# Kernel tuning notes

Measured on AMD Instinct MI355X. Metric: run time of the kernel, lower is better.

Reference implementation:

```python
import jax, jax.numpy as jnp
import numpy as np

B, L, NS, D, M = 64, 200, 1000, 128, 50


def setup_inputs() -> dict:
    key = jax.random.key(0)
    ks = jax.random.split(key, 12)
    s = np.sqrt(2.0 / D).astype(np.float32)  # kaiming_normal scale for Mk/Mv0
    lw = np.sqrt(1.0 / D).astype(np.float32)
    return {
        "skills": jax.random.randint(ks[0], (B, L), 0, NS),
        "responses": jax.random.randint(ks[1], (B, L), 0, 2),
        "k_emb": jax.random.normal(ks[2], (NS, D), jnp.float32) * 0.02,
        "v_emb": jax.random.normal(ks[3], (2 * NS, D), jnp.float32) * 0.02,
        "Mk": jax.random.normal(ks[4], (M, D), jnp.float32) * s,
        "Mv0": jax.random.normal(ks[5], (M, D), jnp.float32) * s,
        "e_W": jax.random.normal(ks[6], (D, D), jnp.float32) * lw,
        "e_b": jnp.zeros((D,), jnp.float32),
        "a_W": jax.random.normal(ks[7], (D, D), jnp.float32) * lw,
        "a_b": jnp.zeros((D,), jnp.float32),
        "f_W": jax.random.normal(ks[8], (D, 2 * D), jnp.float32) * np.sqrt(1.0 / (2 * D)).astype(np.float32),
        "f_b": jnp.zeros((D,), jnp.float32),
        "p_W": jax.random.normal(ks[9], (1, D), jnp.float32) * lw,
        "p_b": jnp.zeros((1,), jnp.float32),
    }


def _dkvmn_forward(skills, responses, k_emb, v_emb, Mk, Mv0,
                   e_W, e_b, a_W, a_b, f_W, f_b, p_W, p_b):
    masked_r = responses * (responses > -1).astype(responses.dtype)
    x = skills + NS * masked_r                      # [B,L] combined (skill,response) id
    k = k_emb[skills]                               # [B,L,D]
    v = v_emb[x]                                    # [B,L,D]
    w = jax.nn.softmax(jnp.einsum('bld,md->blm', k, Mk), axis=-1)  # [B,L,M]
    e = jax.nn.sigmoid(v @ e_W.T + e_b)             # erase  [B,L,D]
    a = jnp.tanh(v @ a_W.T + a_b)                   # add    [B,L,D]

    def step(Mvt, wea):
        wt, et, at = wea                            # [B,M], [B,D], [B,D]
        u = wt[:, :, None]                          # [B,M,1]
        new = Mvt * (1.0 - u * et[:, None, :]) + u * at[:, None, :]
        return new, Mvt                             # emit PRE-update state (Mv[:, :-1])

    Mv_init = jnp.broadcast_to(Mv0[None], (B, M, D))
    _, Mv_pre = jax.lax.scan(
        step, Mv_init,
        (w.transpose(1, 0, 2), e.transpose(1, 0, 2), a.transpose(1, 0, 2)))
    # Mv_pre: [L,B,M,D]; weighted read of pre-update memory
    read = jnp.einsum('blm,lbmd->bld', w, Mv_pre)   # [B,L,D]
    f = jnp.tanh(jnp.concatenate([read, k], axis=-1) @ f_W.T + f_b)  # [B,L,D]
    p = jax.nn.sigmoid(f @ p_W.T + p_b)[..., 0]     # [B,L] (dropout off: eval)
    return p[:, 1:]                                 # pred, [B,L-1]


def reference(skills, responses, k_emb, v_emb, Mk, Mv0,
              e_W, e_b, a_W, a_b, f_W, f_b, p_W, p_b):
    return _dkvmn_forward(skills, responses, k_emb, v_emb, Mk, Mv0,
                          e_W, e_b, a_W, a_b, f_W, f_b, p_W, p_b)
```

## Files before the change

kernel.cpp:

```cpp
#include <hip/hip_runtime.h>
#include <hip/hip_bf16.h>

#define Bb 64
#define Ll 200
#define NSs 1000
#define Dd 128
#define Mm 50

__device__ __forceinline__ float bcast_lane(float v, int l) {
    return __int_as_float(__builtin_amdgcn_readlane(__float_as_int(v), l));
}

__global__ void __launch_bounds__(256) kern_wea(
        const int* __restrict__ skills,
        const int* __restrict__ responses,
        const float* __restrict__ k_emb,
        const float* __restrict__ v_emb,
        const float* __restrict__ Mk,
        const float* __restrict__ e_W, const float* __restrict__ e_b,
        const float* __restrict__ a_W, const float* __restrict__ a_b,
        float* __restrict__ w_out,
        float* __restrict__ e_out, float* __restrict__ a_out) {
    __shared__ float smem[12672];
    int tid = threadIdx.x;

    if (blockIdx.x >= 400) {
        int blk = blockIdx.x - 400;
        float (*mk)[Dd + 4] = (float(*)[Dd + 4])smem;
        float (*kr)[Dd + 4] = (float(*)[Dd + 4])(smem + 6600);

        for (int lin = tid; lin < (Mm * Dd) / 4; lin += 256) {
            float4 f = ((const float4*)Mk)[lin];
            *(float4*)&mk[lin >> 5][(lin & 31) * 4] = f;
        }
        for (int lin = tid; lin < 16 * 32; lin += 256) {
            int r  = lin >> 5;
            int c4 = lin & 31;
            int bl = blk * 16 + r;
            float4 f = ((const float4*)(k_emb + (size_t)skills[bl] * Dd))[c4];
            *(float4*)&kr[r][c4 * 4] = f;
        }
        __syncthreads();

        int wave = tid >> 6, lane = tid & 63;
        int mmr  = (lane < Mm) ? lane : 0;
        float acc[4] = {0.f, 0.f, 0.f, 0.f};
#pragma unroll 2
        for (int q = 0; q < 32; ++q) {
            float4 mkv = *(const float4*)&mk[mmr][q * 4];
#pragma unroll
            for (int i = 0; i < 4; ++i) {
                float4 kv = *(const float4*)&kr[wave * 4 + i][q * 4];
                acc[i] = fmaf(mkv.x, kv.x, acc[i]);
                acc[i] = fmaf(mkv.y, kv.y, acc[i]);
                acc[i] = fmaf(mkv.z, kv.z, acc[i]);
                acc[i] = fmaf(mkv.w, kv.w, acc[i]);
            }
        }
#pragma unroll
        for (int i = 0; i < 4; ++i) {
            float logit = (lane < Mm) ? acc[i] : -1e30f;
            float mx = logit;
            for (int off = 32; off > 0; off >>= 1) mx = fmaxf(mx, __shfl_down(mx, off));
            mx = __shfl(mx, 0);
            float ex = (lane < Mm) ? expf(logit - mx) : 0.f;
            float sm = ex;
            for (int off = 32; off > 0; off >>= 1) sm += __shfl_down(sm, off);
            sm = __shfl(sm, 0);
            int bl = blk * 16 + wave * 4 + i;
            if (lane < Mm) w_out[(size_t)bl * Mm + lane] = ex / sm;
        }
        return;
    }

    int blk = blockIdx.x;
    float (*vt)[Dd + 4] = (float(*)[Dd + 4])smem;
    float (*wt)[Dd + 4] = (float(*)[Dd + 4])(smem + 4224);

#pragma unroll
    for (int i = 0; i < 4; ++i) {
        int lin = i * 256 + tid;
        int r   = lin >> 5;
        int c4  = lin & 31;
        int bl  = blk * 32 + r;
        int rr  = responses[bl];
        int x   = skills[bl] + NSs * ((rr > -1) ? rr : 0);
        float4 f = ((const float4*)(v_emb + (size_t)x * Dd))[c4];
        *(float4*)&vt[r][c4 * 4] = f;
    }
    __syncthreads();

    int wave = tid >> 6, lane = tid & 63;
    int pg = lane >> 3, og = lane & 7;

    for (int s = 0; s < 4; ++s) {
        int base_row = wave * 64 + s * 16;
        bool is_e    = base_row < 128;
        const float* W = is_e ? e_W : a_W;
        int wrow0 = is_e ? base_row : base_row - 128;

#pragma unroll
        for (int i = 0; i < 8; ++i) {
            int lin = i * 64 + lane;
            int r   = lin >> 5;
            int c4  = lin & 31;
            float4 f = ((const float4*)(W + (size_t)(wrow0 + r) * Dd))[c4];
            *(float4*)&wt[wave * 16 + r][c4 * 4] = f;
        }

        float acc[4][2] = {};
#pragma unroll 2
        for (int q = 0; q < 32; ++q) {
            float4 av[4], bv[2];
#pragma unroll
            for (int i = 0; i < 4; ++i) av[i] = *(const float4*)&vt[pg + 8 * i][q * 4];
#pragma unroll
            for (int j = 0; j < 2; ++j) bv[j] = *(const float4*)&wt[wave * 16 + og + 8 * j][q * 4];
#pragma unroll
            for (int i = 0; i < 4; ++i)
#pragma unroll
                for (int j = 0; j < 2; ++j) {
                    acc[i][j] = fmaf(av[i].x, bv[j].x, acc[i][j]);
                    acc[i][j] = fmaf(av[i].y, bv[j].y, acc[i][j]);
                    acc[i][j] = fmaf(av[i].z, bv[j].z, acc[i][j]);
                    acc[i][j] = fmaf(av[i].w, bv[j].w, acc[i][j]);
                }
        }

        float* dst = is_e ? e_out : a_out;
#pragma unroll
        for (int j = 0; j < 2; ++j) {
            int row = wrow0 + og + 8 * j;
            float bias = (is_e ? e_b : a_b)[row];
#pragma unroll
            for (int i = 0; i < 4; ++i) {
                int bl = blk * 32 + pg + 8 * i;
                float v = acc[i][j] + bias;
                dst[(size_t)bl * Dd + row] = is_e ? (1.f / (1.f + expf(-v))) : tanhf(v);
            }
        }
    }
}

#define PQ_LOAD(S, tt) do { int _t = (tt);                                   \
    if (_t < T) { size_t _bl = blBase + _t;                                  \
        w##S = (lane < Mm) ? w_ws[_bl * Mm + lane] : 0.f;                    \
        e##S = e_ws[_bl * Dd + d];  a##S = a_ws[_bl * Dd + d]; } } while (0)

#define PQ_BODY(S) do {                                                      \
    _Pragma("unroll")                                                        \
    for (int m = 0; m < Mm; ++m) {                                           \
        float wm = bcast_lane(w##S, m);                                      \
        float A  = fmaf(-wm, e##S, 1.f);                                     \
        Q[m] = fmaf(A, Q[m], wm * a##S);                                     \
        P[m] *= A; } } while (0)

__global__ void __launch_bounds__(128) kern_scan_pq(
        const float* __restrict__ w_ws,
        const float* __restrict__ e_ws,
        const float* __restrict__ a_ws,
        float* __restrict__ P_ws, float* __restrict__ Q_ws,
        int C, int T) {
    int b = blockIdx.x / C, c = blockIdx.x % C;
    int d = threadIdx.x;
    int lane = d & 63;
    float P[Mm], Q[Mm];
#pragma unroll
    for (int m = 0; m < Mm; ++m) { P[m] = 1.f; Q[m] = 0.f; }

    size_t blBase = (size_t)b * Ll + (size_t)c * T;
    float w0 = 0.f, e0 = 0.f, a0 = 0.f;
    float w1 = 0.f, e1 = 0.f, a1 = 0.f;
    float w2 = 0.f, e2 = 0.f, a2 = 0.f;
    PQ_LOAD(0, 0);
    PQ_LOAD(1, 1);
    for (int tt = 0; tt < T; tt += 3) {
        PQ_LOAD(2, tt + 2);  PQ_BODY(0);
        if (tt + 1 < T) { PQ_LOAD(0, tt + 3);  PQ_BODY(1); }
        if (tt + 2 < T) { PQ_LOAD(1, tt + 4);  PQ_BODY(2); }
    }
    size_t base = ((size_t)(b * C + c)) * (Mm * Dd) + d;
#pragma unroll
    for (int m = 0; m < Mm; ++m) {
        P_ws[base + m * Dd] = P[m];
        Q_ws[base + m * Dd] = Q[m];
    }
}

template <int CC>
__global__ void kern_scan_comb_t(
        const float* __restrict__ Mv0,
        const float* __restrict__ P_ws, const float* __restrict__ Q_ws,
        float* __restrict__ S_ws) {
    int idx = blockIdx.x * 256 + threadIdx.x;
    int b   = idx / (Mm * Dd);
    int md  = idx % (Mm * Dd);
    float Pr[CC - 1], Qr[CC - 1];
#pragma unroll
    for (int c = 0; c < CC - 1; ++c) {
        size_t pq = ((size_t)(b * CC + c)) * (Mm * Dd) + md;
        Pr[c] = P_ws[pq];
        Qr[c] = Q_ws[pq];
    }
    float s = Mv0[md];
#pragma unroll
    for (int c = 0; c < CC - 1; ++c) {
        s = fmaf(Pr[c], s, Qr[c]);
        S_ws[((size_t)(b * (CC - 1) + c)) * (Mm * Dd) + md] = s;
    }
}

#define RD_BODY(S, tt) do {                                                  \
    float acc0 = 0.f, acc1 = 0.f;                                            \
    _Pragma("unroll")                                                        \
    for (int m = 0; m < Mm; m += 2) {                                        \
        float wm0 = bcast_lane(w##S, m);                                     \
        float wm1 = bcast_lane(w##S, m + 1);                                 \
        acc0 = fmaf(wm0, mv[m], acc0);                                       \
        mv[m] = fmaf(wm0, fmaf(-e##S, mv[m], a##S), mv[m]);                  \
        acc1 = fmaf(wm1, mv[m + 1], acc1);                                   \
        mv[m + 1] = fmaf(wm1, fmaf(-e##S, mv[m + 1], a##S), mv[m + 1]);      \
    }                                                                        \
    read_ws[(blBase + (tt)) * Dd + d] = acc0 + acc1;                         \
    } while (0)

__global__ void __launch_bounds__(128) kern_scan_rd(
        const float* __restrict__ Mv0,
        const float* __restrict__ S_ws,
        const float* __restrict__ w_ws,
        const float* __restrict__ e_ws,
        const float* __restrict__ a_ws,
        float* __restrict__ read_ws,
        int C, int T) {
    int b = blockIdx.x / C, c = blockIdx.x % C;
    int d = threadIdx.x;
    int lane = d & 63;
    float mv[Mm];
    if (c == 0) {
#pragma unroll
        for (int m = 0; m < Mm; ++m) mv[m] = Mv0[m * Dd + d];
    } else {
        size_t sb = ((size_t)(b * (C - 1) + (c - 1))) * (Mm * Dd) + d;
#pragma unroll
        for (int m = 0; m < Mm; ++m) mv[m] = S_ws[sb + m * Dd];
    }

    size_t blBase = (size_t)b * Ll + (size_t)c * T;
    float w0 = 0.f, e0 = 0.f, a0 = 0.f;
    float w1 = 0.f, e1 = 0.f, a1 = 0.f;
    float w2 = 0.f, e2 = 0.f, a2 = 0.f;
    PQ_LOAD(0, 0);
    PQ_LOAD(1, 1);
    for (int tt = 0; tt < T; tt += 3) {
        PQ_LOAD(2, tt + 2);  RD_BODY(0, tt);
        if (tt + 1 < T) { PQ_LOAD(0, tt + 3);  RD_BODY(1, tt + 1); }
        if (tt + 2 < T) { PQ_LOAD(1, tt + 4);  RD_BODY(2, tt + 2); }
    }
}

__global__ void __launch_bounds__(256) kern_out(
        const int* __restrict__ skills,
        const float* __restrict__ read_ws,
        const float* __restrict__ k_emb,
        const float* __restrict__ f_W, const float* __restrict__ f_b,
        const float* __restrict__ p_W, const float* __restrict__ p_b,
        float* __restrict__ out) {
    __shared__ float ct[32][2 * Dd + 4];
    __shared__ float wt[4][16][Dd + 4];
    __shared__ float pf[32][8];
    int tid = threadIdx.x;
    int blk = blockIdx.x;

#pragma unroll
    for (int i = 0; i < 8; ++i) {
        int lin = i * 256 + tid;
        int r   = lin >> 6;
        int c4  = lin & 63;
        int idx = blk * 32 + r;
        int b   = idx / (Ll - 1);
        int l   = idx % (Ll - 1) + 1;
        int bl  = b * Ll + l;
        float4 f;
        if (c4 < 32) f = ((const float4*)(read_ws + (size_t)bl * Dd))[c4];
        else         f = ((const float4*)(k_emb + (size_t)skills[bl] * Dd))[c4 - 32];
        *(float4*)&ct[r][c4 * 4] = f;
    }
    ((float*)pf)[tid] = 0.f;
    __syncthreads();

    int wave = tid >> 6, lane = tid & 63;
    int pg = lane >> 3, og = lane & 7;

    float ppart[4] = {0.f, 0.f, 0.f, 0.f};
    for (int sub = 0; sub < 2; ++sub) {
        float acc[4][2] = {};
        for (int h = 0; h < 2; ++h) {
#pragma unroll
            for (int i = 0; i < 8; ++i) {
                int lin = i * 64 + lane;
                int r   = lin >> 5;
                int c4  = lin & 31;
                float4 f = ((const float4*)(f_W +
                            (size_t)(wave * 32 + sub * 16 + r) * (2 * Dd)))[h * 32 + c4];
                *(float4*)&wt[wave][r][c4 * 4] = f;
            }
#pragma unroll 2
            for (int q = 0; q < 32; ++q) {
                int k = h * 128 + q * 4;
                float4 av[4], bv[2];
#pragma unroll
                for (int i = 0; i < 4; ++i) av[i] = *(const float4*)&ct[pg + 8 * i][k];
#pragma unroll
                for (int j = 0; j < 2; ++j) bv[j] = *(const float4*)&wt[wave][og + 8 * j][q * 4];
#pragma unroll
                for (int i = 0; i < 4; ++i)
#pragma unroll
                    for (int j = 0; j < 2; ++j) {
                        acc[i][j] = fmaf(av[i].x, bv[j].x, acc[i][j]);
                        acc[i][j] = fmaf(av[i].y, bv[j].y, acc[i][j]);
                        acc[i][j] = fmaf(av[i].z, bv[j].z, acc[i][j]);
                        acc[i][j] = fmaf(av[i].w, bv[j].w, acc[i][j]);
                    }
            }
        }
#pragma unroll
        for (int j = 0; j < 2; ++j) {
            int row = wave * 32 + sub * 16 + og + 8 * j;
            float fb = f_b[row];
            float pw = p_W[row];
#pragma unroll
            for (int i = 0; i < 4; ++i)
                ppart[i] = fmaf(tanhf(acc[i][j] + fb), pw, ppart[i]);
        }
    }
#pragma unroll
    for (int i = 0; i < 4; ++i) {
        float v = ppart[i];
        for (int off = 4; off > 0; off >>= 1) v += __shfl_down(v, off, 8);
        if (og == 0) pf[pg + 8 * i][wave] = v;
    }
    __syncthreads();
    if (tid < 32) {
        float s = pf[tid][0] + pf[tid][1] + pf[tid][2] + pf[tid][3] + p_b[0];
        out[blk * 32 + tid] = 1.f / (1.f + expf(-s));
    }
}

extern "C" void kernel_launch(void* const* d_in, const int* in_sizes, int n_in,
                              void* d_out, int out_size, void* d_ws, size_t ws_size,
                              hipStream_t stream) {
    const int*   skills    = (const int*)  d_in[0];
    const int*   responses = (const int*)  d_in[1];
    const float* k_emb     = (const float*)d_in[2];
    const float* v_emb     = (const float*)d_in[3];
    const float* Mk        = (const float*)d_in[4];
    const float* Mv0       = (const float*)d_in[5];
    const float* e_W       = (const float*)d_in[6];
    const float* e_b       = (const float*)d_in[7];
    const float* a_W       = (const float*)d_in[8];
    const float* a_b       = (const float*)d_in[9];
    const float* f_W       = (const float*)d_in[10];
    const float* f_b       = (const float*)d_in[11];
    const float* p_W       = (const float*)d_in[12];
    const float* p_b       = (const float*)d_in[13];
    (void)in_sizes; (void)n_in; (void)out_size;

    float* out = (float*)d_out;

    float* ws      = (float*)d_ws;
    float* w_ws    = ws;
    float* e_ws    = w_ws + (size_t)Bb * Ll * Mm;
    float* a_ws    = e_ws + (size_t)Bb * Ll * Dd;
    float* read_ws = a_ws + (size_t)Bb * Ll * Dd;
    float* extra   = read_ws + (size_t)Bb * Ll * Dd;

    const size_t baseF = (size_t)Bb * Ll * Mm + 3 * (size_t)Bb * Ll * Dd;
    const size_t BMD   = (size_t)Bb * Mm * Dd;
    int C = 1;
    const int cands[3] = {8, 5, 2};
    for (int i = 0; i < 3; ++i) {
        size_t need = (baseF + BMD * (3 * (size_t)cands[i] - 1)) * sizeof(float);
        if (ws_size >= need) { C = cands[i]; break; }
    }
    int T = Ll / C;
    float* P_ws = extra;
    float* Q_ws = P_ws + BMD * C;
    float* S_ws = Q_ws + BMD * C;

    kern_wea<<<400 + Bb * Ll / 16, 256, 0, stream>>>(skills, responses, k_emb, v_emb, Mk,
                                                     e_W, e_b, a_W, a_b, w_ws, e_ws, a_ws);
    if (C > 1) {
        kern_scan_pq<<<Bb * C, 128, 0, stream>>>(w_ws, e_ws, a_ws, P_ws, Q_ws, C, T);
        int cgrid = (int)(BMD / 256);
        if      (C == 8) kern_scan_comb_t<8><<<cgrid, 256, 0, stream>>>(Mv0, P_ws, Q_ws, S_ws);
        else if (C == 5) kern_scan_comb_t<5><<<cgrid, 256, 0, stream>>>(Mv0, P_ws, Q_ws, S_ws);
        else             kern_scan_comb_t<2><<<cgrid, 256, 0, stream>>>(Mv0, P_ws, Q_ws, S_ws);
    }
    kern_scan_rd<<<Bb * C, 128, 0, stream>>>(Mv0, S_ws, w_ws, e_ws, a_ws, read_ws, C, T);
    kern_out<<<Bb * (Ll - 1) / 32, 256, 0, stream>>>(skills, read_ws, k_emb,
                                                     f_W, f_b, p_W, p_b, out);
}
```

Baseline: 184.4 us.

## Precompute per-id tables for w, e, a and f_W·k; fold chunk combine into read scan

Instead of computing softmax weights, erase and add vectors for every (b,l) token, the first kernel now computes them once per vocabulary entry (1000 skills, 2000 skill-response ids). It also precomputes the k-half of the output projection per skill. The scans gather rows from these tables by index. The separate chunk-combine kernel is removed, and each read-scan block now applies the preceding chunk P/Q transforms itself. This cuts the GEMM work and one launch, at the cost of redundant combine work in later chunks and a fixed chunk count of 8, which assumes the workspace is large enough.

```diff
diff --git a/kernel.cpp b/kernel.cpp
--- a/kernel.cpp
+++ b/kernel.cpp
@@ -6,44 +6,42 @@
 #define NSs 1000
 #define Dd 128
 #define Mm 50
+#define CCk 8
+#define TT 25
 
 __device__ __forceinline__ float bcast_lane(float v, int l) {
     return __int_as_float(__builtin_amdgcn_readlane(__float_as_int(v), l));
 }
 
-__global__ void __launch_bounds__(256) kern_wea(
-        const int* __restrict__ skills,
-        const int* __restrict__ responses,
+__global__ void __launch_bounds__(256) kern_tab(
         const float* __restrict__ k_emb,
         const float* __restrict__ v_emb,
         const float* __restrict__ Mk,
         const float* __restrict__ e_W, const float* __restrict__ e_b,
         const float* __restrict__ a_W, const float* __restrict__ a_b,
-        float* __restrict__ w_out,
-        float* __restrict__ e_out, float* __restrict__ a_out) {
+        const float* __restrict__ f_W,
+        float* __restrict__ wtab, float* __restrict__ etab,
+        float* __restrict__ atab, float* __restrict__ fktab) {
     __shared__ float smem[12672];
     int tid = threadIdx.x;
-
-    if (blockIdx.x >= 400) {
-        int blk = blockIdx.x - 400;
+    int wave = tid >> 6, lane = tid & 63;
+
+    if (blockIdx.x >= 63 && blockIdx.x < 126) {
+        int sk0 = (blockIdx.x - 63) * 16;
         float (*mk)[Dd + 4] = (float(*)[Dd + 4])smem;
         float (*kr)[Dd + 4] = (float(*)[Dd + 4])(smem + 6600);
-
         for (int lin = tid; lin < (Mm * Dd) / 4; lin += 256) {
             float4 f = ((const float4*)Mk)[lin];
             *(float4*)&mk[lin >> 5][(lin & 31) * 4] = f;
         }
         for (int lin = tid; lin < 16 * 32; lin += 256) {
-            int r  = lin >> 5;
-            int c4 = lin & 31;
-            int bl = blk * 16 + r;
-            float4 f = ((const float4*)(k_emb + (size_t)skills[bl] * Dd))[c4];
+            int r = lin >> 5, c4 = lin & 31;
+            int sk = min(sk0 + r, NSs - 1);
+            float4 f = ((const float4*)(k_emb + (size_t)sk * Dd))[c4];
             *(float4*)&kr[r][c4 * 4] = f;
         }
         __syncthreads();
-
-        int wave = tid >> 6, lane = tid & 63;
-        int mmr  = (lane < Mm) ? lane : 0;
+        int mmr = (lane < Mm) ? lane : 0;
         float acc[4] = {0.f, 0.f, 0.f, 0.f};
 #pragma unroll 2
         for (int q = 0; q < 32; ++q) {
@@ -67,85 +65,124 @@
             float sm = ex;
             for (int off = 32; off > 0; off >>= 1) sm += __shfl_down(sm, off);
             sm = __shfl(sm, 0);
-            int bl = blk * 16 + wave * 4 + i;
-            if (lane < Mm) w_out[(size_t)bl * Mm + lane] = ex / sm;
+            int sk = sk0 + wave * 4 + i;
+            if (sk < NSs && lane < Mm) wtab[(size_t)sk * Mm + lane] = ex / sm;
         }
         return;
     }
 
-    int blk = blockIdx.x;
+    bool is_fk = (blockIdx.x >= 126);
+    int r0 = is_fk ? (blockIdx.x - 126) * 32 : blockIdx.x * 32;
+    int rmax = is_fk ? NSs : 2 * NSs;
+    const float* src = is_fk ? k_emb : v_emb;
+
     float (*vt)[Dd + 4] = (float(*)[Dd + 4])smem;
     float (*wt)[Dd + 4] = (float(*)[Dd + 4])(smem + 4224);
-
 #pragma unroll
     for (int i = 0; i < 4; ++i) {
         int lin = i * 256 + tid;
-        int r   = lin >> 5;
-        int c4  = lin & 31;
-        int bl  = blk * 32 + r;
-        int rr  = responses[bl];
-        int x   = skills[bl] + NSs * ((rr > -1) ? rr : 0);
-        float4 f = ((const float4*)(v_emb + (size_t)x * Dd))[c4];
+        int r = lin >> 5, c4 = lin & 31;
+        int x = min(r0 + r, rmax - 1);
+        float4 f = ((const float4*)(src + (size_t)x * Dd))[c4];
         *(float4*)&vt[r][c4 * 4] = f;
     }
     __syncthreads();
-
-    int wave = tid >> 6, lane = tid & 63;
     int pg = lane >> 3, og = lane & 7;
 
-    for (int s = 0; s < 4; ++s) {
-        int base_row = wave * 64 + s * 16;
-        bool is_e    = base_row < 128;
-        const float* W = is_e ? e_W : a_W;
-        int wrow0 = is_e ? base_row : base_row - 128;
-
-#pragma unroll
-        for (int i = 0; i < 8; ++i) {
-            int lin = i * 64 + lane;
-            int r   = lin >> 5;
-            int c4  = lin & 31;
-            float4 f = ((const float4*)(W + (size_t)(wrow0 + r) * Dd))[c4];
-            *(float4*)&wt[wave * 16 + r][c4 * 4] = f;
-        }
-
-        float acc[4][2] = {};
+    if (is_fk) {
+        for (int sub = 0; sub < 2; ++sub) {
+#pragma unroll
+            for (int i = 0; i < 8; ++i) {
+                int lin = i * 64 + lane;
+                int r = lin >> 5, c4 = lin & 31;
+                int row = wave * 32 + sub * 16 + r;
+                float4 f = ((const float4*)(f_W + (size_t)row * (2 * Dd)))[32 + c4];
+                *(float4*)&wt[wave * 16 + r][c4 * 4] = f;
+            }
+            float acc[4][2] = {};
 #pragma unroll 2
-        for (int q = 0; q < 32; ++q) {
-            float4 av[4], bv[2];
-#pragma unroll
-            for (int i = 0; i < 4; ++i) av[i] = *(const float4*)&vt[pg + 8 * i][q * 4];
-#pragma unroll
-            for (int j = 0; j < 2; ++j) bv[j] = *(const float4*)&wt[wave * 16 + og + 8 * j][q * 4];
-#pragma unroll
-            for (int i = 0; i < 4; ++i)
-#pragma unroll
-                for (int j = 0; j < 2; ++j) {
-                    acc[i][j] = fmaf(av[i].x, bv[j].x, acc[i][j]);
-                    acc[i][j] = fmaf(av[i].y, bv[j].y, acc[i][j]);
-                    acc[i][j] = fmaf(av[i].z, bv[j].z, acc[i][j]);
-                    acc[i][j] = fmaf(av[i].w, bv[j].w, acc[i][j]);
+            for (int q = 0; q < 32; ++q) {
+                float4 av[4], bv[2];
+#pragma unroll
+                for (int i = 0; i < 4; ++i) av[i] = *(const float4*)&vt[pg + 8 * i][q * 4];
+#pragma unroll
+                for (int j = 0; j < 2; ++j) bv[j] = *(const float4*)&wt[wave * 16 + og + 8 * j][q * 4];
+#pragma unroll
+                for (int i = 0; i < 4; ++i)
+#pragma unroll
+                    for (int j = 0; j < 2; ++j) {
+                        acc[i][j] = fmaf(av[i].x, bv[j].x, acc[i][j]);
+                        acc[i][j] = fmaf(av[i].y, bv[j].y, acc[i][j]);
+                        acc[i][j] = fmaf(av[i].z, bv[j].z, acc[i][j]);
+                        acc[i][j] = fmaf(av[i].w, bv[j].w, acc[i][j]);
+                    }
+            }
+#pragma unroll
+            for (int j = 0; j < 2; ++j) {
+                int row = wave * 32 + sub * 16 + og + 8 * j;
+#pragma unroll
+                for (int i = 0; i < 4; ++i) {
+                    int sk = r0 + pg + 8 * i;
+                    if (sk < NSs) fktab[(size_t)sk * Dd + row] = acc[i][j];
                 }
-        }
-
-        float* dst = is_e ? e_out : a_out;
-#pragma unroll
-        for (int j = 0; j < 2; ++j) {
-            int row = wrow0 + og + 8 * j;
-            float bias = (is_e ? e_b : a_b)[row];
-#pragma unroll
-            for (int i = 0; i < 4; ++i) {
-                int bl = blk * 32 + pg + 8 * i;
-                float v = acc[i][j] + bias;
-                dst[(size_t)bl * Dd + row] = is_e ? (1.f / (1.f + expf(-v))) : tanhf(v);
-            }
-        }
-    }
-}
-
-#define PQ_LOAD(S, tt) do { int _t = (tt);                                   \
-    if (_t < T) { size_t _bl = blBase + _t;                                  \
-        w##S = (lane < Mm) ? w_ws[_bl * Mm + lane] : 0.f;                    \
-        e##S = e_ws[_bl * Dd + d];  a##S = a_ws[_bl * Dd + d]; } } while (0)
+            }
+        }
+    } else {
+        for (int s = 0; s < 4; ++s) {
+            int base_row = wave * 64 + s * 16;
+            bool is_e = base_row < 128;
+            const float* W = is_e ? e_W : a_W;
+            int wrow0 = is_e ? base_row : base_row - 128;
+#pragma unroll
+            for (int i = 0; i < 8; ++i) {
+                int lin = i * 64 + lane;
+                int r = lin >> 5, c4 = lin & 31;
+                float4 f = ((const float4*)(W + (size_t)(wrow0 + r) * Dd))[c4];
+                *(float4*)&wt[wave * 16 + r][c4 * 4] = f;
+            }
+            float acc[4][2] = {};
+#pragma unroll 2
+            for (int q = 0; q < 32; ++q) {
+                float4 av[4], bv[2];
+#pragma unroll
+                for (int i = 0; i < 4; ++i) av[i] = *(const float4*)&vt[pg + 8 * i][q * 4];
+#pragma unroll
+                for (int j = 0; j < 2; ++j) bv[j] = *(const float4*)&wt[wave * 16 + og + 8 * j][q * 4];
+#pragma unroll
+                for (int i = 0; i < 4; ++i)
+#pragma unroll
+                    for (int j = 0; j < 2; ++j) {
+                        acc[i][j] = fmaf(av[i].x, bv[j].x, acc[i][j]);
+                        acc[i][j] = fmaf(av[i].y, bv[j].y, acc[i][j]);
+                        acc[i][j] = fmaf(av[i].z, bv[j].z, acc[i][j]);
+                        acc[i][j] = fmaf(av[i].w, bv[j].w, acc[i][j]);
+                    }
+            }
+            float* dst = is_e ? etab : atab;
+#pragma unroll
+            for (int j = 0; j < 2; ++j) {
+                int row = wrow0 + og + 8 * j;
+                float bias = (is_e ? e_b : a_b)[row];
+#pragma unroll
+                for (int i = 0; i < 4; ++i) {
+                    int x = r0 + pg + 8 * i;
+                    if (x < 2 * NSs) {
+                        float v = acc[i][j] + bias;
+                        dst[(size_t)x * Dd + row] = is_e ? (1.f / (1.f + expf(-v))) : tanhf(v);
+                    }
+                }
+            }
+        }
+    }
+}
+
+#define TB_LOAD(S, tt) do { int _t = (tt);                                   \
+    if (_t < TT) {                                                           \
+        int _sk = __shfl(skv, _t);                                           \
+        int _x  = __shfl(xv, _t);                                            \
+        w##S = (lane < Mm) ? wtab[(size_t)_sk * Mm + lane] : 0.f;            \
+        e##S = etab[(size_t)_x * Dd + d];                                    \
+        a##S = atab[(size_t)_x * Dd + d]; } } while (0)
 
 #define PQ_BODY(S) do {                                                      \
     _Pragma("unroll")                                                        \
@@ -154,61 +191,6 @@
         float A  = fmaf(-wm, e##S, 1.f);                                     \
         Q[m] = fmaf(A, Q[m], wm * a##S);                                     \
         P[m] *= A; } } while (0)
-
-__global__ void __launch_bounds__(128) kern_scan_pq(
-        const float* __restrict__ w_ws,
-        const float* __restrict__ e_ws,
-        const float* __restrict__ a_ws,
-        float* __restrict__ P_ws, float* __restrict__ Q_ws,
-        int C, int T) {
-    int b = blockIdx.x / C, c = blockIdx.x % C;
-    int d = threadIdx.x;
-    int lane = d & 63;
-    float P[Mm], Q[Mm];
-#pragma unroll
-    for (int m = 0; m < Mm; ++m) { P[m] = 1.f; Q[m] = 0.f; }
-
-    size_t blBase = (size_t)b * Ll + (size_t)c * T;
-    float w0 = 0.f, e0 = 0.f, a0 = 0.f;
-    float w1 = 0.f, e1 = 0.f, a1 = 0.f;
-    float w2 = 0.f, e2 = 0.f, a2 = 0.f;
-    PQ_LOAD(0, 0);
-    PQ_LOAD(1, 1);
-    for (int tt = 0; tt < T; tt += 3) {
-        PQ_LOAD(2, tt + 2);  PQ_BODY(0);
-        if (tt + 1 < T) { PQ_LOAD(0, tt + 3);  PQ_BODY(1); }
-        if (tt + 2 < T) { PQ_LOAD(1, tt + 4);  PQ_BODY(2); }
-    }
-    size_t base = ((size_t)(b * C + c)) * (Mm * Dd) + d;
-#pragma unroll
-    for (int m = 0; m < Mm; ++m) {
-        P_ws[base + m * Dd] = P[m];
-        Q_ws[base + m * Dd] = Q[m];
-    }
-}
-
-template <int CC>
-__global__ void kern_scan_comb_t(
-        const float* __restrict__ Mv0,
-        const float* __restrict__ P_ws, const float* __restrict__ Q_ws,
-        float* __restrict__ S_ws) {
-    int idx = blockIdx.x * 256 + threadIdx.x;
-    int b   = idx / (Mm * Dd);
-    int md  = idx % (Mm * Dd);
-    float Pr[CC - 1], Qr[CC - 1];
-#pragma unroll
-    for (int c = 0; c < CC - 1; ++c) {
-        size_t pq = ((size_t)(b * CC + c)) * (Mm * Dd) + md;
-        Pr[c] = P_ws[pq];
-        Qr[c] = Q_ws[pq];
-    }
-    float s = Mv0[md];
-#pragma unroll
-    for (int c = 0; c < CC - 1; ++c) {
-        s = fmaf(Pr[c], s, Qr[c]);
-        S_ws[((size_t)(b * (CC - 1) + c)) * (Mm * Dd) + md] = s;
-    }
-}
 
 #define RD_BODY(S, tt) do {                                                  \
     float acc0 = 0.f, acc1 = 0.f;                                            \
@@ -224,66 +206,117 @@
     read_ws[(blBase + (tt)) * Dd + d] = acc0 + acc1;                         \
     } while (0)
 
-__global__ void __launch_bounds__(128) kern_scan_rd(
-        const float* __restrict__ Mv0,
-        const float* __restrict__ S_ws,
-        const float* __restrict__ w_ws,
-        const float* __restrict__ e_ws,
-        const float* __restrict__ a_ws,
-        float* __restrict__ read_ws,
-        int C, int T) {
-    int b = blockIdx.x / C, c = blockIdx.x % C;
+__global__ void __launch_bounds__(128) kern_scan_pq(
+        const int* __restrict__ skills,
+        const int* __restrict__ responses,
+        const float* __restrict__ wtab,
+        const float* __restrict__ etab,
+        const float* __restrict__ atab,
+        float* __restrict__ P_ws, float* __restrict__ Q_ws) {
+    int b = blockIdx.x / (CCk - 1), c = blockIdx.x % (CCk - 1);
     int d = threadIdx.x;
     int lane = d & 63;
-    float mv[Mm];
-    if (c == 0) {
-#pragma unroll
-        for (int m = 0; m < Mm; ++m) mv[m] = Mv0[m * Dd + d];
-    } else {
-        size_t sb = ((size_t)(b * (C - 1) + (c - 1))) * (Mm * Dd) + d;
-#pragma unroll
-        for (int m = 0; m < Mm; ++m) mv[m] = S_ws[sb + m * Dd];
-    }
-
-    size_t blBase = (size_t)b * Ll + (size_t)c * T;
+    size_t blBase = (size_t)b * Ll + (size_t)c * TT;
+
+    int skv = 0, xv = 0;
+    if (lane < TT) {
+        skv = skills[blBase + lane];
+        int rr = responses[blBase + lane];
+        xv = skv + NSs * ((rr > -1) ? rr : 0);
+    }
+
+    float P[Mm], Q[Mm];
+#pragma unroll
+    for (int m = 0; m < Mm; ++m) { P[m] = 1.f; Q[m] = 0.f; }
+
     float w0 = 0.f, e0 = 0.f, a0 = 0.f;
     float w1 = 0.f, e1 = 0.f, a1 = 0.f;
     float w2 = 0.f, e2 = 0.f, a2 = 0.f;
-    PQ_LOAD(0, 0);
-    PQ_LOAD(1, 1);
-    for (int tt = 0; tt < T; tt += 3) {
-        PQ_LOAD(2, tt + 2);  RD_BODY(0, tt);
-        if (tt + 1 < T) { PQ_LOAD(0, tt + 3);  RD_BODY(1, tt + 1); }
-        if (tt + 2 < T) { PQ_LOAD(1, tt + 4);  RD_BODY(2, tt + 2); }
+    TB_LOAD(0, 0);
+    TB_LOAD(1, 1);
+    for (int tt = 0; tt < TT; tt += 3) {
+        TB_LOAD(2, tt + 2);  PQ_BODY(0);
+        if (tt + 1 < TT) { TB_LOAD(0, tt + 3);  PQ_BODY(1); }
+        if (tt + 2 < TT) { TB_LOAD(1, tt + 4);  PQ_BODY(2); }
+    }
+    size_t base = ((size_t)(b * (CCk - 1) + c)) * (Mm * Dd) + d;
+#pragma unroll
+    for (int m = 0; m < Mm; ++m) {
+        P_ws[base + m * Dd] = P[m];
+        Q_ws[base + m * Dd] = Q[m];
+    }
+}
+
+__global__ void __launch_bounds__(128) kern_scan_rd(
+        const int* __restrict__ skills,
+        const int* __restrict__ responses,
+        const float* __restrict__ Mv0,
+        const float* __restrict__ wtab,
+        const float* __restrict__ etab,
+        const float* __restrict__ atab,
+        const float* __restrict__ P_ws, const float* __restrict__ Q_ws,
+        float* __restrict__ read_ws) {
+    int b = blockIdx.x / CCk, c = blockIdx.x % CCk;
+    int d = threadIdx.x;
+    int lane = d & 63;
+    size_t blBase = (size_t)b * Ll + (size_t)c * TT;
+
+    int skv = 0, xv = 0;
+    if (lane < TT) {
+        skv = skills[blBase + lane];
+        int rr = responses[blBase + lane];
+        xv = skv + NSs * ((rr > -1) ? rr : 0);
+    }
+
+    float mv[Mm];
+#pragma unroll
+    for (int m = 0; m < Mm; ++m) mv[m] = Mv0[m * Dd + d];
+    for (int cc = 0; cc < c; ++cc) {
+        size_t base = ((size_t)(b * (CCk - 1) + cc)) * (Mm * Dd) + d;
+#pragma unroll
+        for (int m = 0; m < Mm; ++m)
+            mv[m] = fmaf(P_ws[base + m * Dd], mv[m], Q_ws[base + m * Dd]);
+    }
+
+    float w0 = 0.f, e0 = 0.f, a0 = 0.f;
+    float w1 = 0.f, e1 = 0.f, a1 = 0.f;
+    float w2 = 0.f, e2 = 0.f, a2 = 0.f;
+    TB_LOAD(0, 0);
+    TB_LOAD(1, 1);
+    for (int tt = 0; tt < TT; tt += 3) {
+        TB_LOAD(2, tt + 2);  RD_BODY(0, tt);
+        if (tt + 1 < TT) { TB_LOAD(0, tt + 3);  RD_BODY(1, tt + 1); }
+        if (tt + 2 < TT) { TB_LOAD(1, tt + 4);  RD_BODY(2, tt + 2); }
     }
 }
 
 __global__ void __launch_bounds__(256) kern_out(
         const int* __restrict__ skills,
         const float* __restrict__ read_ws,
-        const float* __restrict__ k_emb,
+        const float* __restrict__ fktab,
         const float* __restrict__ f_W, const float* __restrict__ f_b,
         const float* __restrict__ p_W, const float* __restrict__ p_b,
         float* __restrict__ out) {
-    __shared__ float ct[32][2 * Dd + 4];
+    __shared__ float ct[32][Dd + 4];
+    __shared__ float fkt[32][Dd + 4];
     __shared__ float wt[4][16][Dd + 4];
     __shared__ float pf[32][8];
     int tid = threadIdx.x;
     int blk = blockIdx.x;
 
 #pragma unroll
-    for (int i = 0; i < 8; ++i) {
+    for (int i = 0; i < 4; ++i) {
         int lin = i * 256 + tid;
-        int r   = lin >> 6;
-        int c4  = lin & 63;
+        int r = lin >> 5, c4 = lin & 31;
         int idx = blk * 32 + r;
-        int b   = idx / (Ll - 1);
-        int l   = idx % (Ll - 1) + 1;
-        int bl  = b * Ll + l;
-        float4 f;
-        if (c4 < 32) f = ((const float4*)(read_ws + (size_t)bl * Dd))[c4];
-        else         f = ((const float4*)(k_emb + (size_t)skills[bl] * Dd))[c4 - 32];
+        int b = idx / (Ll - 1);
+        int l = idx % (Ll - 1) + 1;
+        int bl = b * Ll + l;
+        float4 f = ((const float4*)(read_ws + (size_t)bl * Dd))[c4];
         *(float4*)&ct[r][c4 * 4] = f;
+        int sk = skills[bl];
+        float4 g = ((const float4*)(fktab + (size_t)sk * Dd))[c4];
+        *(float4*)&fkt[r][c4 * 4] = g;
     }
     ((float*)pf)[tid] = 0.f;
     __syncthreads();
@@ -294,34 +327,30 @@
     float ppart[4] = {0.f, 0.f, 0.f, 0.f};
     for (int sub = 0; sub < 2; ++sub) {
         float acc[4][2] = {};
-        for (int h = 0; h < 2; ++h) {
-#pragma unroll
-            for (int i = 0; i < 8; ++i) {
-                int lin = i * 64 + lane;
-                int r   = lin >> 5;
-                int c4  = lin & 31;
-                float4 f = ((const float4*)(f_W +
-                            (size_t)(wave * 32 + sub * 16 + r) * (2 * Dd)))[h * 32 + c4];
-                *(float4*)&wt[wave][r][c4 * 4] = f;
-            }
+#pragma unroll
+        for (int i = 0; i < 8; ++i) {
+            int lin = i * 64 + lane;
+            int r = lin >> 5, c4 = lin & 31;
+            int row = wave * 32 + sub * 16 + r;
+            float4 f = ((const float4*)(f_W + (size_t)row * (2 * Dd)))[c4];
+            *(float4*)&wt[wave][r][c4 * 4] = f;
+        }
 #pragma unroll 2
-            for (int q = 0; q < 32; ++q) {
-                int k = h * 128 + q * 4;
-                float4 av[4], bv[2];
-#pragma unroll
-                for (int i = 0; i < 4; ++i) av[i] = *(const float4*)&ct[pg + 8 * i][k];
-#pragma unroll
-                for (int j = 0; j < 2; ++j) bv[j] = *(const float4*)&wt[wave][og + 8 * j][q * 4];
-#pragma unroll
-                for (int i = 0; i < 4; ++i)
-#pragma unroll
-                    for (int j = 0; j < 2; ++j) {
-                        acc[i][j] = fmaf(av[i].x, bv[j].x, acc[i][j]);
-                        acc[i][j] = fmaf(av[i].y, bv[j].y, acc[i][j]);
-                        acc[i][j] = fmaf(av[i].z, bv[j].z, acc[i][j]);
-                        acc[i][j] = fmaf(av[i].w, bv[j].w, acc[i][j]);
-                    }
-            }
+        for (int q = 0; q < 32; ++q) {
+            float4 av[4], bv[2];
+#pragma unroll
+            for (int i = 0; i < 4; ++i) av[i] = *(const float4*)&ct[pg + 8 * i][q * 4];
+#pragma unroll
+            for (int j = 0; j < 2; ++j) bv[j] = *(const float4*)&wt[wave][og + 8 * j][q * 4];
+#pragma unroll
+            for (int i = 0; i < 4; ++i)
+#pragma unroll
+                for (int j = 0; j < 2; ++j) {
+                    acc[i][j] = fmaf(av[i].x, bv[j].x, acc[i][j]);
+                    acc[i][j] = fmaf(av[i].y, bv[j].y, acc[i][j]);
+                    acc[i][j] = fmaf(av[i].z, bv[j].z, acc[i][j]);
+                    acc[i][j] = fmaf(av[i].w, bv[j].w, acc[i][j]);
+                }
         }
 #pragma unroll
         for (int j = 0; j < 2; ++j) {
@@ -329,8 +358,10 @@
             float fb = f_b[row];
             float pw = p_W[row];
 #pragma unroll
-            for (int i = 0; i < 4; ++i)
-                ppart[i] = fmaf(tanhf(acc[i][j] + fb), pw, ppart[i]);
+            for (int i = 0; i < 4; ++i) {
+                float fkv = fkt[pg + 8 * i][row];
+                ppart[i] = fmaf(tanhf(acc[i][j] + fkv + fb), pw, ppart[i]);
+            }
         }
     }
 #pragma unroll
@@ -363,40 +394,28 @@
     const float* f_b       = (const float*)d_in[11];
     const float* p_W       = (const float*)d_in[12];
     const float* p_b       = (const float*)d_in[13];
-    (void)in_sizes; (void)n_in; (void)out_size;
+    (void)in_sizes; (void)n_in; (void)out_size; (void)ws_size;
 
     float* out = (float*)d_out;
 
+    const size_t BLD = (size_t)Bb * Ll * Dd;
+    const size_t BMD = (size_t)Bb * Mm * Dd;
+
     float* ws      = (float*)d_ws;
-    float* w_ws    = ws;
-    float* e_ws    = w_ws + (size_t)Bb * Ll * Mm;
-    float* a_ws    = e_ws + (size_t)Bb * Ll * Dd;
-    float* read_ws = a_ws + (size_t)Bb * Ll * Dd;
-    float* extra   = read_ws + (size_t)Bb * Ll * Dd;
-
-    const size_t baseF = (size_t)Bb * Ll * Mm + 3 * (size_t)Bb * Ll * Dd;
-    const size_t BMD   = (size_t)Bb * Mm * Dd;
-    int C = 1;
-    const int cands[3] = {8, 5, 2};
-    for (int i = 0; i < 3; ++i) {
-        size_t need = (baseF + BMD * (3 * (size_t)cands[i] - 1)) * sizeof(float);
-        if (ws_size >= need) { C = cands[i]; break; }
-    }
-    int T = Ll / C;
-    float* P_ws = extra;
-    float* Q_ws = P_ws + BMD * C;
-    float* S_ws = Q_ws + BMD * C;
-
-    kern_wea<<<400 + Bb * Ll / 16, 256, 0, stream>>>(skills, responses, k_emb, v_emb, Mk,
-                                                     e_W, e_b, a_W, a_b, w_ws, e_ws, a_ws);
-    if (C > 1) {
-        kern_scan_pq<<<Bb * C, 128, 0, stream>>>(w_ws, e_ws, a_ws, P_ws, Q_ws, C, T);
-        int cgrid = (int)(BMD / 256);
-        if      (C == 8) kern_scan_comb_t<8><<<cgrid, 256, 0, stream>>>(Mv0, P_ws, Q_ws, S_ws);
-        else if (C == 5) kern_scan_comb_t<5><<<cgrid, 256, 0, stream>>>(Mv0, P_ws, Q_ws, S_ws);
-        else             kern_scan_comb_t<2><<<cgrid, 256, 0, stream>>>(Mv0, P_ws, Q_ws, S_ws);
-    }
-    kern_scan_rd<<<Bb * C, 128, 0, stream>>>(Mv0, S_ws, w_ws, e_ws, a_ws, read_ws, C, T);
-    kern_out<<<Bb * (Ll - 1) / 32, 256, 0, stream>>>(skills, read_ws, k_emb,
+    float* read_ws = ws;
+    float* P_ws    = read_ws + BLD;
+    float* Q_ws    = P_ws + (CCk - 1) * BMD;
+    float* wtab    = Q_ws + (CCk - 1) * BMD;
+    float* etab    = wtab + (size_t)NSs * Mm;
+    float* atab    = etab + (size_t)2 * NSs * Dd;
+    float* fktab   = atab + (size_t)2 * NSs * Dd;
+
+    kern_tab<<<158, 256, 0, stream>>>(k_emb, v_emb, Mk, e_W, e_b, a_W, a_b, f_W,
+                                      wtab, etab, atab, fktab);
+    kern_scan_pq<<<Bb * (CCk - 1), 128, 0, stream>>>(skills, responses,
+                                                     wtab, etab, atab, P_ws, Q_ws);
+    kern_scan_rd<<<Bb * CCk, 128, 0, stream>>>(skills, responses, Mv0,
+                                               wtab, etab, atab, P_ws, Q_ws, read_ws);
+    kern_out<<<Bb * (Ll - 1) / 32, 256, 0, stream>>>(skills, read_ws, fktab,
                                                      f_W, f_b, p_W, p_b, out);
 }
```

Result: no change. 181.3 us (-1.7%).
